# Kernel optimization log

Hardware: AMD Instinct MI355X
Metric: run time of the kernel (lower is better)

The kernel has to match this reference:

```python
import jax, jax.numpy as jnp
import numpy as np

HEADS = 20


def _sdpa(q, k, v):
    # q: [B,H,Sq,D], k/v: [B,H,Sk,D]
    scale = 1.0 / jnp.sqrt(jnp.asarray(q.shape[-1], q.dtype))
    scores = jnp.einsum('bhqd,bhkd->bhqk', q, k) * scale
    probs = jax.nn.softmax(scores, axis=-1)
    return jnp.einsum('bhqk,bhkd->bhqd', probs, v)


def _split_heads(x, B, H):
    # [B,S,H*D] -> [B,H,S,D]
    S = x.shape[1]
    D = x.shape[2] // H
    return x.reshape(B, S, H, D).transpose(0, 2, 1, 3)


def setup_inputs() -> dict:
    key = jax.random.key(0)
    ks = jax.random.split(key, 10)
    B, S, C = 4, 4096, 1280
    T, Lid, X = 77, 32, 2048
    sc = lambda fan_in: 1.0 / np.sqrt(fan_in)
    return {
        'hidden_states': jax.random.normal(ks[0], (B, S, C), jnp.float32),
        'encoder_hidden_states': jax.random.normal(ks[1], (B, T, X), jnp.float32),
        'id_embedding': jax.random.normal(ks[2], (B, Lid, X), jnp.float32),
        'Wq': jax.random.normal(ks[3], (C, C), jnp.float32) * sc(C),
        'Wk': jax.random.normal(ks[4], (C, X), jnp.float32) * sc(X),
        'Wv': jax.random.normal(ks[5], (C, X), jnp.float32) * sc(X),
        'Wik': jax.random.normal(ks[6], (C, X), jnp.float32) * sc(X),
        'Wiv': jax.random.normal(ks[7], (C, X), jnp.float32) * sc(X),
        'Wo': jax.random.normal(ks[8], (C, C), jnp.float32) * sc(C),
        'bo': jnp.zeros((C,), jnp.float32),
    }


def reference(hidden_states, encoder_hidden_states, id_embedding,
              Wq, Wk, Wv, Wik, Wiv, Wo, bo):
    id_scale = 1.0
    B, S, C = hidden_states.shape
    H = HEADS
    residual = hidden_states

    q = _split_heads(hidden_states @ Wq.T, B, H)              # [B,H,S,D]
    k = _split_heads(encoder_hidden_states @ Wk.T, B, H)      # [B,H,T,D]
    v = _split_heads(encoder_hidden_states @ Wv.T, B, H)

    cross = _sdpa(q, k, v)                                    # [B,H,S,D]

    id_k = _split_heads(id_embedding @ Wik.T, B, H)           # [B,H,Lid,D]
    id_v = _split_heads(id_embedding @ Wiv.T, B, H)
    id_out = _sdpa(q, id_k, id_v)                             # [B,H,S,D]

    combined = cross + id_scale * id_out
    combined = combined.transpose(0, 2, 1, 3).reshape(B, S, C)

    out = combined @ Wo.T + bo
    out = out + residual  # residual_connection=True, rescale_output_factor=1.0
    return out
```

## Files before the change

### kernel.cpp

```cpp
#include <hip/hip_runtime.h>

typedef short short8 __attribute__((ext_vector_type(8)));
typedef unsigned short ushort8 __attribute__((ext_vector_type(8)));
typedef float float4v __attribute__((ext_vector_type(4)));

__device__ __forceinline__ unsigned short f2bf(float f) {
    union { float f; unsigned u; } v; v.f = f;
    unsigned r = v.u + 0x7fffu + ((v.u >> 16) & 1u);
    return (unsigned short)(r >> 16);
}

__device__ __forceinline__ void async_copy16(const void* g, void* l) {
    __builtin_amdgcn_global_load_lds(
        (__attribute__((address_space(1))) void*)g,
        (__attribute__((address_space(3))) void*)l,
        16, 0, 0);
}

__global__ __launch_bounds__(256) void cast_bf16_kernel(
        const float* __restrict__ in, unsigned short* __restrict__ out, int n) {
    int i4 = (blockIdx.x * 256 + threadIdx.x) * 4;
    if (i4 < n) {
        float4 f = *(const float4*)(in + i4);
        ushort4 u;
        u.x = f2bf(f.x); u.y = f2bf(f.y); u.z = f2bf(f.z); u.w = f2bf(f.w);
        *(ushort4*)(out + i4) = u;
    }
}

__global__ __launch_bounds__(256) void cast_enc_pad_kernel(
        const float* __restrict__ in, unsigned short* __restrict__ out) {
    int i4 = blockIdx.x * 256 + threadIdx.x;
    if (i4 < 4 * 77 * 2048 / 4) {
        const int per_b = 77 * 2048 / 4;
        int b = i4 / per_b;
        int rem = i4 - b * per_b;
        float4 f = *(const float4*)(in + (size_t)i4 * 4);
        ushort4 u;
        u.x = f2bf(f.x); u.y = f2bf(f.y); u.z = f2bf(f.z); u.w = f2bf(f.w);
        *(ushort4*)(out + ((size_t)b * (96 * 2048 / 4) + rem) * 4) = u;
    }
}

struct CastBatch {
    const float* src[8];
    unsigned short* dst[8];
    int n[8];
};
__global__ __launch_bounds__(256) void cast_batch_kernel(CastBatch cb) {
    const int t = blockIdx.y;
    const int n = cb.n[t];
    int i4 = (blockIdx.x * 256 + threadIdx.x) * 4;
    if (i4 < n) {
        float4 f = *(const float4*)(cb.src[t] + i4);
        ushort4 u;
        u.x = f2bf(f.x); u.y = f2bf(f.y); u.z = f2bf(f.z); u.w = f2bf(f.w);
        *(ushort4*)(cb.dst[t] + i4) = u;
    }
}

template<int EPI>
__device__ __forceinline__ void gemm_core(
        const unsigned short* __restrict__ A,
        const unsigned short* __restrict__ B,
        float* __restrict__ Cf,
        unsigned short* __restrict__ Cb,
        const float* __restrict__ bias,
        const float* __restrict__ resid,
        int Mclamp, int N, int K, int bm, int bn) {
    __shared__ unsigned short As[128 * 64];
    __shared__ unsigned short Bs[128 * 64];

    const int tid  = threadIdx.x;
    const int lane = tid & 63;
    const int wave = tid >> 6;
    const int wm   = (wave >> 1) * 64;
    const int wn   = (wave & 1) * 64;
    const int lr   = lane & 15;
    const int lq   = lane >> 4;

    float4v acc[4][4] = {};

    const unsigned short* aptr[4];
    const unsigned short* bptr[4];
    #pragma unroll
    for (int r = 0; r < 4; ++r) {
        const int linear = r * 256 + tid;
        const int row = linear >> 3;
        const int c = (linear & 7) ^ (row & 7);
        int ar = bm + row; if (ar >= Mclamp) ar = Mclamp - 1;
        aptr[r] = A + (size_t)ar * K + c * 8;
        bptr[r] = B + (size_t)(bn + row) * K + c * 8;
    }

    for (int ks = 0; ks < K; ks += 64) {
        #pragma unroll
        for (int r = 0; r < 4; ++r) {
            async_copy16(aptr[r] + ks, (char*)As + (size_t)(r * 256 + tid) * 16);
            async_copy16(bptr[r] + ks, (char*)Bs + (size_t)(r * 256 + tid) * 16);
        }
        __syncthreads();

        #pragma unroll
        for (int kw = 0; kw < 2; ++kw) {
            short8 af[4], bfr[4];
            #pragma unroll
            for (int i = 0; i < 4; ++i) {
                const int row = wm + i * 16 + lr;
                af[i] = *(const short8*)(As + row * 64 + (((kw << 2) | lq) ^ (row & 7)) * 8);
            }
            #pragma unroll
            for (int j = 0; j < 4; ++j) {
                const int row = wn + j * 16 + lr;
                bfr[j] = *(const short8*)(Bs + row * 64 + (((kw << 2) | lq) ^ (row & 7)) * 8);
            }
            #pragma unroll
            for (int i = 0; i < 4; ++i)
                #pragma unroll
                for (int j = 0; j < 4; ++j)
                    acc[i][j] = __builtin_amdgcn_mfma_f32_16x16x32_bf16(
                                    af[i], bfr[j], acc[i][j], 0, 0, 0);
        }
        __syncthreads();
    }

    #pragma unroll
    for (int i = 0; i < 4; ++i) {
        #pragma unroll
        for (int r = 0; r < 4; ++r) {
            const int row = bm + wm + i * 16 + lq * 4 + r;
            const size_t base = (size_t)row * N;
            #pragma unroll
            for (int j = 0; j < 4; ++j) {
                const int col = bn + wn + j * 16 + lr;
                const float v = acc[i][j][r];
                const size_t idx = base + col;
                if (EPI == 2)      Cf[idx] = v + bias[col] + resid[idx];
                else if (EPI == 1) Cb[idx] = f2bf(v);
                else               Cf[idx] = v;
            }
        }
    }
}

__global__ __launch_bounds__(256) void gemm_kv4_kernel(
        const unsigned short* __restrict__ Aenc,
        const unsigned short* __restrict__ Aid,
        const unsigned short* __restrict__ Wk,
        const unsigned short* __restrict__ Wv,
        const unsigned short* __restrict__ Wik,
        const unsigned short* __restrict__ Wiv,
        unsigned short* __restrict__ Kb, unsigned short* __restrict__ Vb,
        unsigned short* __restrict__ IKb, unsigned short* __restrict__ IVb,
        int N, int K) {
    const int z = blockIdx.z;
    const int bm = blockIdx.x * 128;
    const int Mrows = (z < 2) ? 384 : 128;
    if (bm >= Mrows) return;
    const unsigned short* A = (z < 2) ? Aenc : Aid;
    const unsigned short* B = (z == 0) ? Wk : (z == 1) ? Wv : (z == 2) ? Wik : Wiv;
    unsigned short* C = (z == 0) ? Kb : (z == 1) ? Vb : (z == 2) ? IKb : IVb;
    gemm_core<1>(A, B, nullptr, C, nullptr, nullptr, Mrows, N, K,
                 bm, blockIdx.y * 128);
}

template<int EPI>
__global__ __launch_bounds__(512) void gemm256_kernel(
        const unsigned short* __restrict__ A,
        const unsigned short* __restrict__ B,
        float* __restrict__ Cf,
        unsigned short* __restrict__ Cb,
        const float* __restrict__ bias,
        const float* __restrict__ resid,
        int N, int K, int tn) {
    __shared__ unsigned short As[2][256 * 64];
    __shared__ unsigned short Bs[2][256 * 64];

    const int tid  = threadIdx.x;
    const int lane = tid & 63;
    const int wave = tid >> 6;
    const int wm   = (wave >> 2) * 128;
    const int wn   = (wave & 3) * 64;
    const int l15  = lane & 15;
    const int lq   = lane >> 4;

    int wg = blockIdx.x;
    const int q = gridDim.x >> 3;
    wg = (wg & 7) * q + (wg >> 3);
    const int mt = wg / tn;
    const int nt = wg - mt * tn;
    const int bm = mt * 256;
    const int bn = nt * 256;

    float4v acc[8][4] = {};

    const unsigned short* aptr[4];
    const unsigned short* bptr[4];
    #pragma unroll
    for (int r = 0; r < 4; ++r) {
        const int linear = r * 512 + tid;
        const int row = linear >> 3;
        const int c = (linear & 7) ^ (row & 7);
        aptr[r] = A + (size_t)(bm + row) * K + c * 8;
        bptr[r] = B + (size_t)(bn + row) * K + c * 8;
    }

    auto stage = [&](int ks, int b) {
        #pragma unroll
        for (int r = 0; r < 4; ++r)
            async_copy16(aptr[r] + ks, (char*)&As[b][0] + (r * 512 + tid) * 16);
        #pragma unroll
        for (int r = 0; r < 4; ++r)
            async_copy16(bptr[r] + ks, (char*)&Bs[b][0] + (r * 512 + tid) * 16);
    };

    const int NT = K >> 6;
    stage(0, 0);
    stage(64, 1);

    for (int t = 0; t < NT; ++t) {
        const int cur = t & 1;
        if (t == NT - 1) {
            asm volatile("s_waitcnt vmcnt(0)" ::: "memory");
        } else {
            asm volatile("s_waitcnt vmcnt(8)" ::: "memory");
        }
        __builtin_amdgcn_s_barrier();
        __builtin_amdgcn_sched_barrier(0);

        short8 a0[8], b0[4], a1[8], b1[4];
        #pragma unroll
        for (int i = 0; i < 8; ++i) {
            const int row = wm + i * 16 + l15;
            a0[i] = *(const short8*)(&As[cur][row * 64 + ((lq ^ (row & 7)) << 3)]);
        }
        #pragma unroll
        for (int j = 0; j < 4; ++j) {
            const int row = wn + j * 16 + l15;
            b0[j] = *(const short8*)(&Bs[cur][row * 64 + ((lq ^ (row & 7)) << 3)]);
        }
        #pragma unroll
        for (int i = 0; i < 8; ++i)
            #pragma unroll
            for (int j = 0; j < 4; ++j)
                acc[i][j] = __builtin_amdgcn_mfma_f32_16x16x32_bf16(
                                a0[i], b0[j], acc[i][j], 0, 0, 0);
        #pragma unroll
        for (int i = 0; i < 8; ++i) {
            const int row = wm + i * 16 + l15;
            a1[i] = *(const short8*)(&As[cur][row * 64 + (((4 | lq) ^ (row & 7)) << 3)]);
        }
        #pragma unroll
        for (int j = 0; j < 4; ++j) {
            const int row = wn + j * 16 + l15;
            b1[j] = *(const short8*)(&Bs[cur][row * 64 + (((4 | lq) ^ (row & 7)) << 3)]);
        }
        asm volatile("s_waitcnt lgkmcnt(0)" ::: "memory");
        __builtin_amdgcn_sched_barrier(0);
        if (t < NT - 2) {
            __builtin_amdgcn_s_barrier();
            stage((t + 2) << 6, cur);
        }
        __builtin_amdgcn_s_setprio(1);
        #pragma unroll
        for (int i = 0; i < 8; ++i)
            #pragma unroll
            for (int j = 0; j < 4; ++j)
                acc[i][j] = __builtin_amdgcn_mfma_f32_16x16x32_bf16(
                                a1[i], b1[j], acc[i][j], 0, 0, 0);
        __builtin_amdgcn_s_setprio(0);
    }

    #pragma unroll
    for (int i = 0; i < 8; ++i) {
        #pragma unroll
        for (int r = 0; r < 4; ++r) {
            const int row = bm + wm + i * 16 + lq * 4 + r;
            const size_t base = (size_t)row * N;
            #pragma unroll
            for (int j = 0; j < 4; ++j) {
                const int col = bn + wn + j * 16 + l15;
                const float v = acc[i][j][r];
                const size_t idx = base + col;
                if (EPI == 2)      Cf[idx] = v + bias[col] + resid[idx];
                else if (EPI == 1) Cb[idx] = f2bf(v);
                else               Cf[idx] = v;
            }
        }
    }
}

#define VT_STRIDE 136
__global__ __launch_bounds__(256) void attn_mfma_kernel(
        const unsigned short* __restrict__ Q,
        const unsigned short* __restrict__ Kb,
        const unsigned short* __restrict__ Vb,
        const unsigned short* __restrict__ IKb,
        const unsigned short* __restrict__ IVb,
        unsigned short* __restrict__ Cmb) {
    const int b = blockIdx.z;
    const int h = blockIdx.y;
    const int hoff = h * 64;
    const int qbase = blockIdx.x * 64;
    const int tid = threadIdx.x;
    const int lane = tid & 63;
    const int wave = tid >> 6;
    const int l15 = lane & 15;
    const int quad = lane >> 4;

    __shared__ unsigned short Vt[64 * VT_STRIDE];
    __shared__ unsigned short Pl[64 * VT_STRIDE];

    for (int i = tid; i < 96 * 8; i += 256) {
        const int c = i / 96;
        const int key = i - c * 96;
        short8 v = *(const short8*)(Vb + (size_t)(b * 96 + key) * 1280 + hoff + c * 8);
        #pragma unroll
        for (int j = 0; j < 8; ++j)
            Vt[(c * 8 + j) * VT_STRIDE + key] = (unsigned short)v[j];
    }
    {
        const int c = tid >> 5;
        const int key = tid & 31;
        short8 v = *(const short8*)(IVb + (size_t)(b * 32 + key) * 1280 + hoff + c * 8);
        #pragma unroll
        for (int j = 0; j < 8; ++j)
            Vt[(c * 8 + j) * VT_STRIDE + 96 + key] = (unsigned short)v[j];
    }
    __syncthreads();

    const int qrow = b * 4096 + qbase + wave * 16 + l15;
    const unsigned short* qp = Q + (size_t)qrow * 1280 + hoff + quad * 8;
    const short8 aQ0 = *(const short8*)(qp);
    const short8 aQ1 = *(const short8*)(qp + 32);

    const float scale = 0.125f;
    float lC[4] = {0.f, 0.f, 0.f, 0.f};
    float lI[4] = {0.f, 0.f, 0.f, 0.f};

    #pragma unroll
    for (int t = 0; t < 5; ++t) {
        const unsigned short* kp = Kb + (size_t)(b * 96 + t * 16 + l15) * 1280 + hoff + quad * 8;
        const short8 bK0 = *(const short8*)(kp);
        const short8 bK1 = *(const short8*)(kp + 32);
        float4v s = {};
        s = __builtin_amdgcn_mfma_f32_16x16x32_bf16(aQ0, bK0, s, 0, 0, 0);
        s = __builtin_amdgcn_mfma_f32_16x16x32_bf16(aQ1, bK1, s, 0, 0, 0);
        #pragma unroll
        for (int r = 0; r < 4; ++r) {
            float p = __expf(s[r] * scale);
            if (t == 4 && l15 >= 13) p = 0.f;
            lC[r] += p;
            Pl[(wave * 16 + quad * 4 + r) * VT_STRIDE + t * 16 + l15] = f2bf(p);
        }
    }
    #pragma unroll
    for (int r = 0; r < 4; ++r)
        Pl[(wave * 16 + quad * 4 + r) * VT_STRIDE + 80 + l15] = 0;

    #pragma unroll
    for (int t = 0; t < 2; ++t) {
        const unsigned short* kp = IKb + (size_t)(b * 32 + t * 16 + l15) * 1280 + hoff + quad * 8;
        const short8 bK0 = *(const short8*)(kp);
        const short8 bK1 = *(const short8*)(kp + 32);
        float4v s = {};
        s = __builtin_amdgcn_mfma_f32_16x16x32_bf16(aQ0, bK0, s, 0, 0, 0);
        s = __builtin_amdgcn_mfma_f32_16x16x32_bf16(aQ1, bK1, s, 0, 0, 0);
        #pragma unroll
        for (int r = 0; r < 4; ++r) {
            const float p = __expf(s[r] * scale);
            lI[r] += p;
            Pl[(wave * 16 + quad * 4 + r) * VT_STRIDE + 96 + t * 16 + l15] = f2bf(p);
        }
    }

    #pragma unroll
    for (int m = 1; m <= 8; m <<= 1) {
        #pragma unroll
        for (int r = 0; r < 4; ++r) {
            lC[r] += __shfl_xor(lC[r], m);
            lI[r] += __shfl_xor(lI[r], m);
        }
    }
    __syncthreads();

    float4v oC[4] = {};
    float4v oI[4] = {};
    #pragma unroll
    for (int kt = 0; kt < 3; ++kt) {
        const short8 aP = *(const short8*)(Pl + (wave * 16 + l15) * VT_STRIDE + kt * 32 + quad * 8);
        #pragma unroll
        for (int td = 0; td < 4; ++td) {
            const short8 bV = *(const short8*)(Vt + (td * 16 + l15) * VT_STRIDE + kt * 32 + quad * 8);
            oC[td] = __builtin_amdgcn_mfma_f32_16x16x32_bf16(aP, bV, oC[td], 0, 0, 0);
        }
    }
    {
        const short8 aP = *(const short8*)(Pl + (wave * 16 + l15) * VT_STRIDE + 96 + quad * 8);
        #pragma unroll
        for (int td = 0; td < 4; ++td) {
            const short8 bV = *(const short8*)(Vt + (td * 16 + l15) * VT_STRIDE + 96 + quad * 8);
            oI[td] = __builtin_amdgcn_mfma_f32_16x16x32_bf16(aP, bV, oI[td], 0, 0, 0);
        }
    }

    float rc[4], ri[4];
    #pragma unroll
    for (int r = 0; r < 4; ++r) { rc[r] = 1.f / lC[r]; ri[r] = 1.f / lI[r]; }

    #pragma unroll
    for (int td = 0; td < 4; ++td) {
        #pragma unroll
        for (int r = 0; r < 4; ++r) {
            const int row = b * 4096 + qbase + wave * 16 + quad * 4 + r;
            const int col = hoff + td * 16 + l15;
            Cmb[(size_t)row * 1280 + col] = f2bf(oC[td][r] * rc[r] + oI[td][r] * ri[r]);
        }
    }
}

extern "C" void kernel_launch(void* const* d_in, const int* in_sizes, int n_in,
                              void* d_out, int out_size, void* d_ws, size_t ws_size,
                              hipStream_t stream) {
    const float* hs  = (const float*)d_in[0];
    const float* enc = (const float*)d_in[1];
    const float* idm = (const float*)d_in[2];
    const float* Wq  = (const float*)d_in[3];
    const float* Wk  = (const float*)d_in[4];
    const float* Wv  = (const float*)d_in[5];
    const float* Wik = (const float*)d_in[6];
    const float* Wiv = (const float*)d_in[7];
    const float* Wo  = (const float*)d_in[8];
    const float* bo  = (const float*)d_in[9];
    float* out = (float*)d_out;

    char* ws = (char*)d_ws;
    size_t off = 0;
    auto carve = [&](size_t bytes) {
        char* p = ws + off;
        off += (bytes + 255) & ~(size_t)255;
        return p;
    };

    unsigned short* Xh   = (unsigned short*)carve(16384ULL * 1280 * 2);
    unsigned short* Wq_b = (unsigned short*)carve(1280ULL * 1280 * 2);
    unsigned short* Wk_b = (unsigned short*)carve(1280ULL * 2048 * 2);
    unsigned short* Wv_b = (unsigned short*)carve(1280ULL * 2048 * 2);
    unsigned short* Wik_b= (unsigned short*)carve(1280ULL * 2048 * 2);
    unsigned short* Wiv_b= (unsigned short*)carve(1280ULL * 2048 * 2);
    unsigned short* Wo_b = (unsigned short*)carve(1280ULL * 1280 * 2);
    unsigned short* Encb = (unsigned short*)carve(384ULL * 2048 * 2);
    unsigned short* Idb  = (unsigned short*)carve(128ULL * 2048 * 2);
    unsigned short* Qb   = (unsigned short*)carve(16384ULL * 1280 * 2);
    unsigned short* Kb   = (unsigned short*)carve(384ULL * 1280 * 2);
    unsigned short* Vb   = (unsigned short*)carve(384ULL * 1280 * 2);
    unsigned short* IKb  = (unsigned short*)carve(128ULL * 1280 * 2);
    unsigned short* IVb  = (unsigned short*)carve(128ULL * 1280 * 2);
    (void)ws_size; (void)in_sizes; (void)n_in; (void)out_size;

    cast_bf16_kernel<<<(4 * 4096 * 1280 / 4 + 255) / 256, 256, 0, stream>>>(
        hs, Xh, 4 * 4096 * 1280);
    cast_enc_pad_kernel<<<(4 * 77 * 2048 / 4 + 255) / 256, 256, 0, stream>>>(enc, Encb);

    CastBatch cb;
    cb.src[0] = Wq;  cb.dst[0] = Wq_b;  cb.n[0] = 1280 * 1280;
    cb.src[1] = Wk;  cb.dst[1] = Wk_b;  cb.n[1] = 1280 * 2048;
    cb.src[2] = Wv;  cb.dst[2] = Wv_b;  cb.n[2] = 1280 * 2048;
    cb.src[3] = Wik; cb.dst[3] = Wik_b; cb.n[3] = 1280 * 2048;
    cb.src[4] = Wiv; cb.dst[4] = Wiv_b; cb.n[4] = 1280 * 2048;
    cb.src[5] = Wo;  cb.dst[5] = Wo_b;  cb.n[5] = 1280 * 1280;
    cb.src[6] = idm; cb.dst[6] = Idb;   cb.n[6] = 4 * 32 * 2048;
    cb.src[7] = nullptr; cb.dst[7] = nullptr; cb.n[7] = 0;
    cast_batch_kernel<<<dim3((1280 * 2048 / 4 + 255) / 256, 7), 256, 0, stream>>>(cb);

    gemm256_kernel<1><<<dim3(64 * 5), 512, 0, stream>>>(
        Xh, Wq_b, nullptr, Qb, nullptr, nullptr, 1280, 1280, 5);

    gemm_kv4_kernel<<<dim3(3, 10, 4), 256, 0, stream>>>(
        Encb, Idb, Wk_b, Wv_b, Wik_b, Wiv_b, Kb, Vb, IKb, IVb, 1280, 2048);

    attn_mfma_kernel<<<dim3(64, 20, 4), 256, 0, stream>>>(Qb, Kb, Vb, IKb, IVb, Xh);

    gemm256_kernel<2><<<dim3(64 * 5), 512, 0, stream>>>(
        Xh, Wo_b, out, nullptr, bo, hs, 1280, 1280, 5);
}
```

Measured before the change: 467.7 us.

## Restructure 256x256 GEMM mainloop into 4-slot K=32 ring with split A/B staging

```diff
diff --git a/kernel.cpp b/kernel.cpp
--- a/kernel.cpp
+++ b/kernel.cpp
@@ -173,8 +173,8 @@
         const float* __restrict__ bias,
         const float* __restrict__ resid,
         int N, int K, int tn) {
-    __shared__ unsigned short As[2][256 * 64];
-    __shared__ unsigned short Bs[2][256 * 64];
+    __shared__ unsigned short Ar[4][256 * 32];
+    __shared__ unsigned short Br[4][256 * 32];
 
     const int tid  = threadIdx.x;
     const int lane = tid & 63;
@@ -194,81 +194,92 @@
 
     float4v acc[8][4] = {};
 
-    const unsigned short* aptr[4];
-    const unsigned short* bptr[4];
-    #pragma unroll
-    for (int r = 0; r < 4; ++r) {
-        const int linear = r * 512 + tid;
-        const int row = linear >> 3;
-        const int c = (linear & 7) ^ (row & 7);
-        aptr[r] = A + (size_t)(bm + row) * K + c * 8;
-        bptr[r] = B + (size_t)(bn + row) * K + c * 8;
-    }
-
-    auto stage = [&](int ks, int b) {
-        #pragma unroll
-        for (int r = 0; r < 4; ++r)
-            async_copy16(aptr[r] + ks, (char*)&As[b][0] + (r * 512 + tid) * 16);
-        #pragma unroll
-        for (int r = 0; r < 4; ++r)
-            async_copy16(bptr[r] + ks, (char*)&Bs[b][0] + (r * 512 + tid) * 16);
+    const unsigned short* aS[2];
+    const unsigned short* bS[2];
+    int dOff[2];
+    #pragma unroll
+    for (int g = 0; g < 2; ++g) {
+        const int d = g * 512 + tid;
+        const int row = d >> 2;
+        const int cl = (d & 3) ^ ((row >> 1) & 3);
+        aS[g] = A + (size_t)(bm + row) * K + cl * 8;
+        bS[g] = B + (size_t)(bn + row) * K + cl * 8;
+        dOff[g] = d * 16;
+    }
+
+    auto stageA = [&](int sj) {
+        const int s = sj & 3;
+        #pragma unroll
+        for (int g = 0; g < 2; ++g)
+            async_copy16(aS[g] + sj * 32, (char*)&Ar[s][0] + dOff[g]);
     };
-
-    const int NT = K >> 6;
-    stage(0, 0);
-    stage(64, 1);
-
-    for (int t = 0; t < NT; ++t) {
-        const int cur = t & 1;
-        if (t == NT - 1) {
-            asm volatile("s_waitcnt vmcnt(0)" ::: "memory");
-        } else {
-            asm volatile("s_waitcnt vmcnt(8)" ::: "memory");
-        }
+    auto stageB = [&](int sj) {
+        const int s = sj & 3;
+        #pragma unroll
+        for (int g = 0; g < 2; ++g)
+            async_copy16(bS[g] + sj * 32, (char*)&Br[s][0] + dOff[g]);
+    };
+
+    const int NSLOT = K >> 5;
+    stageA(0); stageB(0); stageA(1); stageB(1); stageA(2); stageB(2);
+    asm volatile("s_waitcnt vmcnt(8)" ::: "memory");
+    __builtin_amdgcn_s_barrier();
+    __builtin_amdgcn_sched_barrier(0);
+
+    for (int j = 0; j < NSLOT; ++j) {
+        const int s = j & 3;
+        const unsigned short* As_ = &Ar[s][0];
+        const unsigned short* Bs_ = &Br[s][0];
+        short8 af0[4], af1[4], bf[4];
+
+        #pragma unroll
+        for (int ii = 0; ii < 4; ++ii) {
+            const int row = wm + ii * 16 + l15;
+            af0[ii] = *(const short8*)(As_ + row * 32 + ((lq ^ ((row >> 1) & 3)) << 3));
+        }
+        #pragma unroll
+        for (int j2 = 0; j2 < 4; ++j2) {
+            const int row = wn + j2 * 16 + l15;
+            bf[j2] = *(const short8*)(Bs_ + row * 32 + ((lq ^ ((row >> 1) & 3)) << 3));
+        }
+        if (j + 3 < NSLOT) stageA(j + 3);
+        __builtin_amdgcn_s_barrier();
+        asm volatile("s_waitcnt lgkmcnt(0)" ::: "memory");
+        __builtin_amdgcn_sched_barrier(0);
+        __builtin_amdgcn_s_setprio(1);
+        #pragma unroll
+        for (int ii = 0; ii < 4; ++ii)
+            #pragma unroll
+            for (int j2 = 0; j2 < 4; ++j2)
+                acc[ii][j2] = __builtin_amdgcn_mfma_f32_16x16x32_bf16(
+                                  af0[ii], bf[j2], acc[ii][j2], 0, 0, 0);
+        __builtin_amdgcn_s_setprio(0);
         __builtin_amdgcn_s_barrier();
         __builtin_amdgcn_sched_barrier(0);
 
-        short8 a0[8], b0[4], a1[8], b1[4];
-        #pragma unroll
-        for (int i = 0; i < 8; ++i) {
-            const int row = wm + i * 16 + l15;
-            a0[i] = *(const short8*)(&As[cur][row * 64 + ((lq ^ (row & 7)) << 3)]);
-        }
-        #pragma unroll
-        for (int j = 0; j < 4; ++j) {
-            const int row = wn + j * 16 + l15;
-            b0[j] = *(const short8*)(&Bs[cur][row * 64 + ((lq ^ (row & 7)) << 3)]);
-        }
-        #pragma unroll
-        for (int i = 0; i < 8; ++i)
-            #pragma unroll
-            for (int j = 0; j < 4; ++j)
-                acc[i][j] = __builtin_amdgcn_mfma_f32_16x16x32_bf16(
-                                a0[i], b0[j], acc[i][j], 0, 0, 0);
-        #pragma unroll
-        for (int i = 0; i < 8; ++i) {
-            const int row = wm + i * 16 + l15;
-            a1[i] = *(const short8*)(&As[cur][row * 64 + (((4 | lq) ^ (row & 7)) << 3)]);
-        }
-        #pragma unroll
-        for (int j = 0; j < 4; ++j) {
-            const int row = wn + j * 16 + l15;
-            b1[j] = *(const short8*)(&Bs[cur][row * 64 + (((4 | lq) ^ (row & 7)) << 3)]);
-        }
+        #pragma unroll
+        for (int ii = 0; ii < 4; ++ii) {
+            const int row = wm + 64 + ii * 16 + l15;
+            af1[ii] = *(const short8*)(As_ + row * 32 + ((lq ^ ((row >> 1) & 3)) << 3));
+        }
+        if (j + 3 < NSLOT) stageB(j + 3);
+        __builtin_amdgcn_s_barrier();
         asm volatile("s_waitcnt lgkmcnt(0)" ::: "memory");
         __builtin_amdgcn_sched_barrier(0);
-        if (t < NT - 2) {
-            __builtin_amdgcn_s_barrier();
-            stage((t + 2) << 6, cur);
-        }
         __builtin_amdgcn_s_setprio(1);
         #pragma unroll
-        for (int i = 0; i < 8; ++i)
-            #pragma unroll
-            for (int j = 0; j < 4; ++j)
-                acc[i][j] = __builtin_amdgcn_mfma_f32_16x16x32_bf16(
-                                a1[i], b1[j], acc[i][j], 0, 0, 0);
+        for (int ii = 0; ii < 4; ++ii)
+            #pragma unroll
+            for (int j2 = 0; j2 < 4; ++j2)
+                acc[4 + ii][j2] = __builtin_amdgcn_mfma_f32_16x16x32_bf16(
+                                      af1[ii], bf[j2], acc[4 + ii][j2], 0, 0, 0);
         __builtin_amdgcn_s_setprio(0);
+
+        if (j <= NSLOT - 4)      { asm volatile("s_waitcnt vmcnt(8)" ::: "memory"); }
+        else if (j == NSLOT - 3) { asm volatile("s_waitcnt vmcnt(4)" ::: "memory"); }
+        else if (j <  NSLOT - 1) { asm volatile("s_waitcnt vmcnt(0)" ::: "memory"); }
+        __builtin_amdgcn_s_barrier();
+        __builtin_amdgcn_sched_barrier(0);
     }
 
     #pragma unroll
```

Result: slower. 495.3 us (+5.9%).
